# Kernel tuning notes

Measured on AMD Instinct MI355X. Metric: run time of the kernel, lower is better.

The kernel has to match this reference:

```python
import math
import jax, jax.numpy as jnp
import numpy as np

B, H, HKV, L, S, D = 1, 32, 8, 2048, 2048, 128
N_REP = H // HKV          # 4
SCALE = 1.0 / math.sqrt(D)


def setup_inputs() -> dict:
    key = jax.random.key(0)
    k1, k2, k3, k4 = jax.random.split(key, 4)
    query = jax.random.normal(k1, (B, H, L, D), dtype=jnp.float32)
    k_ = jax.random.normal(k2, (B, HKV, S, D), dtype=jnp.float32)
    v_ = jax.random.normal(k3, (B, HKV, S, D), dtype=jnp.float32)
    attn_mask = jax.random.normal(k4, (B, 1, L, S), dtype=jnp.float32)
    return {"query": query, "key": k_, "value": v_, "attn_mask": attn_mask}


def reference(query, key, value, attn_mask):
    # repeat_kv: Q -> [B, HKV, n_rep, L, D]; K/V stay [B, HKV, S, D]
    # (the torch code reshapes K/V to [B, HKV, 1, S, D]; broadcasting via
    # einsum is equivalent), mask unsqueezed at dim 1 -> [B, 1, 1, L, S].
    q = query.reshape(B, HKV, N_REP, L, D)
    scores = jnp.einsum("bkrld,bksd->bkrls", q, key)          # [B,HKV,n_rep,L,S]
    scores = scores + attn_mask[:, None]                        # broadcast add
    # softmax_fp8(x, dim=-1, invAttnHead=1/sqrt(D)) scales input by invAttnHead
    w = jax.nn.softmax(scores * SCALE, axis=-1)
    # dropout_p = 0.0 -> identity
    out = jnp.einsum("bkrls,bksd->bkrld", w, value)             # [B,HKV,n_rep,L,D]
    return out
```

## Files before the change

kernel.cpp:

```cpp
#include <hip/hip_runtime.h>

#define NH   32
#define NKV  8
#define LQ   2048
#define SK   2048
#define DH   128
#define BM   128
#define BN   64
#define KSTRIDE 136
#define VSTRIDE 72
#define PSTRIDE 72

typedef __attribute__((ext_vector_type(8)))  short bf8;
typedef __attribute__((ext_vector_type(4)))  float f4;
typedef __attribute__((ext_vector_type(16))) float f16v;

#if __has_builtin(__builtin_amdgcn_exp2f)
#define EXP2F(x) __builtin_amdgcn_exp2f(x)
#else
#define EXP2F(x) exp2f(x)
#endif

__device__ __forceinline__ unsigned short f2bf(float f) {
    unsigned int u = __builtin_bit_cast(unsigned int, f);
    u = (u + 0x7FFFu + ((u >> 16) & 1u)) >> 16;
    return (unsigned short)u;
}

__global__ __launch_bounds__(256) void convert_k_kernel(
    const float* __restrict__ K, unsigned short* __restrict__ Kb)
{
    size_t base = ((size_t)blockIdx.x * 256 + threadIdx.x) * 8;
    float4 a = *(const float4*)(K + base);
    float4 b = *(const float4*)(K + base + 4);
    bf8 o;
    o[0] = (short)f2bf(a.x); o[1] = (short)f2bf(a.y);
    o[2] = (short)f2bf(a.z); o[3] = (short)f2bf(a.w);
    o[4] = (short)f2bf(b.x); o[5] = (short)f2bf(b.y);
    o[6] = (short)f2bf(b.z); o[7] = (short)f2bf(b.w);
    *(bf8*)(Kb + base) = o;
}

__global__ __launch_bounds__(256) void transpose_v_kernel(
    const float* __restrict__ V, unsigned short* __restrict__ VTb)
{
    __shared__ __align__(16) unsigned short Vl[DH * VSTRIDE];
    const int tid = threadIdx.x;
    const int kv  = blockIdx.x >> 5;
    const int s0  = (blockIdx.x & 31) * 64;
    const float* Vh = V + (size_t)kv * SK * DH;

    #pragma unroll
    for (int i = 0; i < 8; ++i) {
        int idx = tid * 4 + i * 1024;
        int s = idx >> 7, d = idx & 127;
        const float4 v4 = *(const float4*)(Vh + (size_t)(s0 + s) * DH + d);
        Vl[(d + 0) * VSTRIDE + s] = f2bf(v4.x);
        Vl[(d + 1) * VSTRIDE + s] = f2bf(v4.y);
        Vl[(d + 2) * VSTRIDE + s] = f2bf(v4.z);
        Vl[(d + 3) * VSTRIDE + s] = f2bf(v4.w);
    }
    __syncthreads();
    unsigned short* out = VTb + (size_t)kv * DH * SK;
    #pragma unroll
    for (int i = 0; i < 4; ++i) {
        int c = tid + i * 256;
        int d = c >> 3, s8 = (c & 7) * 8;
        *(bf8*)(out + (size_t)d * SK + s0 + s8) = *(const bf8*)(Vl + d * VSTRIDE + s8);
    }
}

__global__ __launch_bounds__(256, 2) void fattn_kernel(
    const float* __restrict__ Q, const unsigned short* __restrict__ Kb,
    const unsigned short* __restrict__ VTb, const float* __restrict__ M,
    float* __restrict__ O)
{
    __shared__ __align__(16) unsigned short Klds[BN * KSTRIDE];
    __shared__ __align__(16) unsigned short Vlds[DH * VSTRIDE];
    __shared__ __align__(16) unsigned short Plds[4 * 32 * PSTRIDE];

    const int tid  = threadIdx.x;
    const int wave = tid >> 6;
    const int lane = tid & 63;
    const int l32  = lane & 31;
    const int hh   = lane >> 5;

    const int bx = blockIdx.x;
    const int h  = bx >> 4;
    const int lt = bx & 15;
    const int q0 = lt * BM;
    const int kv = h >> 2;

    const float*          Qh  = Q   + (size_t)h  * LQ * DH;
    const unsigned short* Kh  = Kb  + (size_t)kv * SK * DH;
    const unsigned short* VTh = VTb + (size_t)kv * DH * SK;

    const int sK0 = tid >> 4,        dK0 = (tid & 15) * 8;
    const int dV0 = tid >> 3,        sV0 = (tid & 7) * 8;

    const int qrow = q0 + wave * 32 + l32;
    const float* Mq = M + (size_t)qrow * SK;

    bf8 bQ[8];
    #pragma unroll
    for (int ks = 0; ks < 8; ++ks) {
        const float* qp = Qh + (size_t)qrow * DH + ks * 16 + hh * 8;
        float4 a = *(const float4*)(qp);
        float4 b = *(const float4*)(qp + 4);
        bQ[ks][0] = (short)f2bf(a.x); bQ[ks][1] = (short)f2bf(a.y);
        bQ[ks][2] = (short)f2bf(a.z); bQ[ks][3] = (short)f2bf(a.w);
        bQ[ks][4] = (short)f2bf(b.x); bQ[ks][5] = (short)f2bf(b.y);
        bQ[ks][6] = (short)f2bf(b.z); bQ[ks][7] = (short)f2bf(b.w);
    }

    f16v accO[4];
    #pragma unroll
    for (int nt = 0; nt < 4; ++nt)
        #pragma unroll
        for (int r = 0; r < 16; ++r) accO[nt][r] = 0.f;
    float lpart = 0.f;

    const float scale_log2e = 0.08838834764831845f * 1.4426950408889634f;

    unsigned short* Pw = Plds + wave * 32 * PSTRIDE;

    bf8 kf[4], vf[4];
    #pragma unroll
    for (int c = 0; c < 4; ++c) {
        kf[c] = *(const bf8*)(Kh + (size_t)(sK0 + c * 16) * DH + dK0);
        vf[c] = *(const bf8*)(VTh + (size_t)(dV0 + c * 32) * SK + sV0);
    }

    for (int s0i = 0; s0i < SK; s0i += BN) {
        __syncthreads();
        #pragma unroll
        for (int c = 0; c < 4; ++c) {
            *(bf8*)(Klds + (sK0 + c * 16) * KSTRIDE + dK0) = kf[c];
            *(bf8*)(Vlds + (dV0 + c * 32) * VSTRIDE + sV0) = vf[c];
        }
        __syncthreads();
        if (s0i + BN < SK) {
            #pragma unroll
            for (int c = 0; c < 4; ++c) {
                kf[c] = *(const bf8*)(Kh + (size_t)(s0i + BN + sK0 + c * 16) * DH + dK0);
                vf[c] = *(const bf8*)(VTh + (size_t)(dV0 + c * 32) * SK + s0i + BN + sV0);
            }
        }
        float4 mv[2][4];
        #pragma unroll
        for (int mt = 0; mt < 2; ++mt)
            #pragma unroll
            for (int grp = 0; grp < 4; ++grp)
                mv[mt][grp] = *(const float4*)(Mq + s0i + mt * 32 + grp * 8 + hh * 4);

        f16v accS[2];
        #pragma unroll
        for (int mt = 0; mt < 2; ++mt) {
            f16v a;
            #pragma unroll
            for (int r = 0; r < 16; ++r) a[r] = 0.f;
            #pragma unroll
            for (int ks = 0; ks < 8; ++ks) {
                bf8 aK = *(const bf8*)(Klds + (mt * 32 + l32) * KSTRIDE + ks * 16 + hh * 8);
                a = __builtin_amdgcn_mfma_f32_32x32x16_bf16(aK, bQ[ks], a, 0, 0, 0);
            }
            accS[mt] = a;
        }

        #pragma unroll
        for (int mt = 0; mt < 2; ++mt) {
            #pragma unroll
            for (int grp = 0; grp < 4; ++grp) {
                ushort4 pk;
                float e0 = EXP2F((accS[mt][grp * 4 + 0] + mv[mt][grp].x) * scale_log2e);
                float e1 = EXP2F((accS[mt][grp * 4 + 1] + mv[mt][grp].y) * scale_log2e);
                float e2 = EXP2F((accS[mt][grp * 4 + 2] + mv[mt][grp].z) * scale_log2e);
                float e3 = EXP2F((accS[mt][grp * 4 + 3] + mv[mt][grp].w) * scale_log2e);
                lpart += (e0 + e1) + (e2 + e3);
                pk.x = f2bf(e0); pk.y = f2bf(e1); pk.z = f2bf(e2); pk.w = f2bf(e3);
                *(ushort4*)(Pw + l32 * PSTRIDE + mt * 32 + grp * 8 + hh * 4) = pk;
            }
        }
        asm volatile("s_waitcnt lgkmcnt(0)" ::: "memory");

        bf8 bP[4];
        #pragma unroll
        for (int ks = 0; ks < 4; ++ks)
            bP[ks] = *(const bf8*)(Pw + l32 * PSTRIDE + ks * 16 + hh * 8);
        #pragma unroll
        for (int nt = 0; nt < 4; ++nt) {
            f16v a = accO[nt];
            #pragma unroll
            for (int ks = 0; ks < 4; ++ks) {
                bf8 aV = *(const bf8*)(Vlds + (nt * 32 + l32) * VSTRIDE + ks * 16 + hh * 8);
                a = __builtin_amdgcn_mfma_f32_32x32x16_bf16(aV, bP[ks], a, 0, 0, 0);
            }
            accO[nt] = a;
        }
    }

    float l = lpart + __shfl_xor(lpart, 32);
    float inv = 1.0f / l;
    float* Op = O + (size_t)h * LQ * DH + (size_t)qrow * DH;
    #pragma unroll
    for (int nt = 0; nt < 4; ++nt) {
        #pragma unroll
        for (int grp = 0; grp < 4; ++grp) {
            int d = nt * 32 + grp * 8 + hh * 4;
            float4 o;
            o.x = accO[nt][grp * 4 + 0] * inv;
            o.y = accO[nt][grp * 4 + 1] * inv;
            o.z = accO[nt][grp * 4 + 2] * inv;
            o.w = accO[nt][grp * 4 + 3] * inv;
            *(float4*)(Op + d) = o;
        }
    }
}

extern "C" void kernel_launch(void* const* d_in, const int* in_sizes, int n_in,
                              void* d_out, int out_size, void* d_ws, size_t ws_size,
                              hipStream_t stream) {
    const float* Q = (const float*)d_in[0];
    const float* K = (const float*)d_in[1];
    const float* V = (const float*)d_in[2];
    const float* M = (const float*)d_in[3];
    float* O = (float*)d_out;

    unsigned short* Kb  = (unsigned short*)d_ws;
    unsigned short* VTb = Kb + (size_t)NKV * SK * DH;

    convert_k_kernel<<<dim3((NKV * SK * DH) / (256 * 8)), 256, 0, stream>>>(K, Kb);
    transpose_v_kernel<<<dim3(NKV * (SK / 64)), 256, 0, stream>>>(V, VTb);

    dim3 grid(NH * (LQ / BM));
    fattn_kernel<<<grid, 256, 0, stream>>>(Q, Kb, VTb, M, O);
}
```

Measured before the change: 199.8 us.

## Rework attention kernel with async LDS double-buffering, swizzled layouts, register P

```diff
diff --git a/kernel.cpp b/kernel.cpp
--- a/kernel.cpp
+++ b/kernel.cpp
@@ -7,13 +7,12 @@
 #define DH   128
 #define BM   128
 #define BN   64
-#define KSTRIDE 136
+#define NT   (SK / BN)
 #define VSTRIDE 72
-#define PSTRIDE 72
 
 typedef __attribute__((ext_vector_type(8)))  short bf8;
-typedef __attribute__((ext_vector_type(4)))  float f4;
 typedef __attribute__((ext_vector_type(16))) float f16v;
+typedef __attribute__((ext_vector_type(4)))  unsigned int u32x4;
 
 #if __has_builtin(__builtin_amdgcn_exp2f)
 #define EXP2F(x) __builtin_amdgcn_exp2f(x)
@@ -27,18 +26,34 @@
     return (unsigned short)u;
 }
 
+__device__ __forceinline__ unsigned int cvtpk_bf16(float lo, float hi) {
+    unsigned int r;
+    asm("v_cvt_pk_bf16_f32 %0, %1, %2" : "=v"(r) : "v"(lo), "v"(hi));
+    return r;
+}
+
+#define GLOAD_LDS16(g, l)                                                      \
+    __builtin_amdgcn_global_load_lds(                                          \
+        (const __attribute__((address_space(1))) void*)(g),                    \
+        (__attribute__((address_space(3))) void*)(l), 16, 0, 0)
+
 __global__ __launch_bounds__(256) void convert_k_kernel(
     const float* __restrict__ K, unsigned short* __restrict__ Kb)
 {
-    size_t base = ((size_t)blockIdx.x * 256 + threadIdx.x) * 8;
-    float4 a = *(const float4*)(K + base);
-    float4 b = *(const float4*)(K + base + 4);
+    unsigned int cid = blockIdx.x * 256 + threadIdx.x;
+    unsigned int p   = cid & 15;
+    unsigned int row = cid >> 4;
+    unsigned int s   = row & (SK - 1);
+    unsigned int c   = p ^ (s & 15);
+    const float* src = K + (size_t)row * DH + c * 8;
+    float4 a = *(const float4*)(src);
+    float4 b = *(const float4*)(src + 4);
     bf8 o;
     o[0] = (short)f2bf(a.x); o[1] = (short)f2bf(a.y);
     o[2] = (short)f2bf(a.z); o[3] = (short)f2bf(a.w);
     o[4] = (short)f2bf(b.x); o[5] = (short)f2bf(b.y);
     o[6] = (short)f2bf(b.z); o[7] = (short)f2bf(b.w);
-    *(bf8*)(Kb + base) = o;
+    *(bf8*)(Kb + (size_t)row * DH + p * 8) = o;
 }
 
 __global__ __launch_bounds__(256) void transpose_v_kernel(
@@ -47,7 +62,8 @@
     __shared__ __align__(16) unsigned short Vl[DH * VSTRIDE];
     const int tid = threadIdx.x;
     const int kv  = blockIdx.x >> 5;
-    const int s0  = (blockIdx.x & 31) * 64;
+    const int t   = blockIdx.x & 31;
+    const int s0  = t * 64;
     const float* Vh = V + (size_t)kv * SK * DH;
 
     #pragma unroll
@@ -61,12 +77,13 @@
         Vl[(d + 3) * VSTRIDE + s] = f2bf(v4.w);
     }
     __syncthreads();
-    unsigned short* out = VTb + (size_t)kv * DH * SK;
+    unsigned short* out = VTb + (size_t)(kv * 32 + t) * (DH * 64);
     #pragma unroll
     for (int i = 0; i < 4; ++i) {
         int c = tid + i * 256;
-        int d = c >> 3, s8 = (c & 7) * 8;
-        *(bf8*)(out + (size_t)d * SK + s0 + s8) = *(const bf8*)(Vl + d * VSTRIDE + s8);
+        int d = c >> 3, p = c & 7;
+        int sc = (p ^ (d & 7)) * 8;
+        *(bf8*)(out + d * 64 + p * 8) = *(const bf8*)(Vl + d * VSTRIDE + sc);
     }
 }
 
@@ -75,144 +92,212 @@
     const unsigned short* __restrict__ VTb, const float* __restrict__ M,
     float* __restrict__ O)
 {
-    __shared__ __align__(16) unsigned short Klds[BN * KSTRIDE];
-    __shared__ __align__(16) unsigned short Vlds[DH * VSTRIDE];
-    __shared__ __align__(16) unsigned short Plds[4 * 32 * PSTRIDE];
+    __shared__ __align__(1024) unsigned char smem[65536];
+    unsigned char* KB = smem;
+    unsigned char* VB = smem + 32768;
 
     const int tid  = threadIdx.x;
     const int wave = tid >> 6;
     const int lane = tid & 63;
     const int l32  = lane & 31;
     const int hh   = lane >> 5;
-
-    const int bx = blockIdx.x;
+    const int qg   = wave >> 1;
+    const int sg   = wave & 1;
+
+    const int bx = ((int)blockIdx.x & 7) * 64 + ((int)blockIdx.x >> 3);
     const int h  = bx >> 4;
     const int lt = bx & 15;
     const int q0 = lt * BM;
     const int kv = h >> 2;
 
-    const float*          Qh  = Q   + (size_t)h  * LQ * DH;
-    const unsigned short* Kh  = Kb  + (size_t)kv * SK * DH;
-    const unsigned short* VTh = VTb + (size_t)kv * DH * SK;
-
-    const int sK0 = tid >> 4,        dK0 = (tid & 15) * 8;
-    const int dV0 = tid >> 3,        sV0 = (tid & 7) * 8;
-
-    const int qrow = q0 + wave * 32 + l32;
-    const float* Mq = M + (size_t)qrow * SK;
-
-    bf8 bQ[8];
-    #pragma unroll
-    for (int ks = 0; ks < 8; ++ks) {
-        const float* qp = Qh + (size_t)qrow * DH + ks * 16 + hh * 8;
-        float4 a = *(const float4*)(qp);
-        float4 b = *(const float4*)(qp + 4);
-        bQ[ks][0] = (short)f2bf(a.x); bQ[ks][1] = (short)f2bf(a.y);
-        bQ[ks][2] = (short)f2bf(a.z); bQ[ks][3] = (short)f2bf(a.w);
-        bQ[ks][4] = (short)f2bf(b.x); bQ[ks][5] = (short)f2bf(b.y);
-        bQ[ks][6] = (short)f2bf(b.z); bQ[ks][7] = (short)f2bf(b.w);
-    }
-
-    f16v accO[4];
-    #pragma unroll
-    for (int nt = 0; nt < 4; ++nt)
-        #pragma unroll
-        for (int r = 0; r < 16; ++r) accO[nt][r] = 0.f;
-    float lpart = 0.f;
-
-    const float scale_log2e = 0.08838834764831845f * 1.4426950408889634f;
-
-    unsigned short* Pw = Plds + wave * 32 * PSTRIDE;
-
-    bf8 kf[4], vf[4];
-    #pragma unroll
-    for (int c = 0; c < 4; ++c) {
-        kf[c] = *(const bf8*)(Kh + (size_t)(sK0 + c * 16) * DH + dK0);
-        vf[c] = *(const bf8*)(VTh + (size_t)(dV0 + c * 32) * SK + sV0);
-    }
-
-    for (int s0i = 0; s0i < SK; s0i += BN) {
-        __syncthreads();
-        #pragma unroll
-        for (int c = 0; c < 4; ++c) {
-            *(bf8*)(Klds + (sK0 + c * 16) * KSTRIDE + dK0) = kf[c];
-            *(bf8*)(Vlds + (dV0 + c * 32) * VSTRIDE + sV0) = vf[c];
-        }
-        __syncthreads();
-        if (s0i + BN < SK) {
-            #pragma unroll
-            for (int c = 0; c < 4; ++c) {
-                kf[c] = *(const bf8*)(Kh + (size_t)(s0i + BN + sK0 + c * 16) * DH + dK0);
-                vf[c] = *(const bf8*)(VTh + (size_t)(dV0 + c * 32) * SK + s0i + BN + sV0);
+    const float* Qh = Q + (size_t)h * LQ * DH;
+    const unsigned char* Kg = (const unsigned char*)(Kb  + (size_t)kv * SK * DH);
+    const unsigned char* Vg = (const unsigned char*)(VTb + (size_t)kv * SK * DH);
+
+    const int qrow0 = q0 + qg * 64 + l32;
+    const float* Mq0 = M + (size_t)qrow0 * SK;
+    const float* Mq1 = Mq0 + (size_t)32 * SK;
+
+    bf8 bQ[2][8];
+    #pragma unroll
+    for (int qt = 0; qt < 2; ++qt) {
+        const float* qp = Qh + (size_t)(qrow0 + qt * 32) * DH + hh * 8;
+        #pragma unroll
+        for (int ks = 0; ks < 8; ++ks) {
+            float4 a = *(const float4*)(qp + ks * 16);
+            float4 b = *(const float4*)(qp + ks * 16 + 4);
+            bf8 o;
+            o[0] = (short)f2bf(a.x); o[1] = (short)f2bf(a.y);
+            o[2] = (short)f2bf(a.z); o[3] = (short)f2bf(a.w);
+            o[4] = (short)f2bf(b.x); o[5] = (short)f2bf(b.y);
+            o[6] = (short)f2bf(b.z); o[7] = (short)f2bf(b.w);
+            bQ[qt][ks] = o;
+        }
+    }
+
+    const int krowz = (sg * 32 + l32) * 256 + ((hh * 16) ^ ((l32 & 15) << 4));
+    const int vrowz = l32 * 128 + ((sg * 64 + hh * 16) ^ ((l32 & 7) << 4));
+
+    const int stoff = wave * 4096 + lane * 16;
+
+    f16v accO[4][2];
+    #pragma unroll
+    for (int dt = 0; dt < 4; ++dt)
+        #pragma unroll
+        for (int qt = 0; qt < 2; ++qt)
+            #pragma unroll
+            for (int r = 0; r < 16; ++r) accO[dt][qt][r] = 0.f;
+    float lp0 = 0.f, lp1 = 0.f;
+    const float cl2e = 0.08838834764831845f * 1.4426950408889634f;
+
+    #pragma unroll
+    for (int c = 0; c < 4; ++c) GLOAD_LDS16(Kg + stoff + c * 1024, KB + stoff + c * 1024);
+    #pragma unroll
+    for (int c = 0; c < 4; ++c) GLOAD_LDS16(Vg + stoff + c * 1024, VB + stoff + c * 1024);
+
+    for (int t = 0; t < NT; ++t) {
+        const int cur = t & 1;
+
+        const float* mp0 = Mq0 + t * 64 + sg * 32 + hh * 4;
+        const float* mp1 = Mq1 + t * 64 + sg * 32 + hh * 4;
+        float4 mv0[4], mv1[4];
+        #pragma unroll
+        for (int g = 0; g < 4; ++g) mv0[g] = *(const float4*)(mp0 + g * 8);
+        #pragma unroll
+        for (int g = 0; g < 4; ++g) mv1[g] = *(const float4*)(mp1 + g * 8);
+        __builtin_amdgcn_sched_barrier(0);
+
+        {
+            const int tn = (t + 1) & (NT - 1);
+            const unsigned char* ksrc = Kg + (size_t)tn * 16384 + stoff;
+            const unsigned char* vsrc = Vg + (size_t)tn * 16384 + stoff;
+            unsigned char* kdst = KB + (cur ^ 1) * 16384 + stoff;
+            unsigned char* vdst = VB + (cur ^ 1) * 16384 + stoff;
+            #pragma unroll
+            for (int c = 0; c < 4; ++c) GLOAD_LDS16(ksrc + c * 1024, kdst + c * 1024);
+            #pragma unroll
+            for (int c = 0; c < 4; ++c) GLOAD_LDS16(vsrc + c * 1024, vdst + c * 1024);
+        }
+        __builtin_amdgcn_sched_barrier(0);
+        asm volatile("s_waitcnt vmcnt(16)" ::: "memory");
+        __builtin_amdgcn_s_barrier();
+        asm volatile("" ::: "memory");
+
+        const unsigned char* kb = KB + cur * 16384;
+        f16v s0, s1;
+        #pragma unroll
+        for (int r = 0; r < 16; ++r) { s0[r] = 0.f; s1[r] = 0.f; }
+        __builtin_amdgcn_s_setprio(1);
+        #pragma unroll
+        for (int ks = 0; ks < 8; ++ks) {
+            bf8 aK = *(const bf8*)(kb + (krowz ^ (ks << 5)));
+            s0 = __builtin_amdgcn_mfma_f32_32x32x16_bf16(aK, bQ[0][ks], s0, 0, 0, 0);
+            s1 = __builtin_amdgcn_mfma_f32_32x32x16_bf16(aK, bQ[1][ks], s1, 0, 0, 0);
+        }
+        __builtin_amdgcn_s_setprio(0);
+
+        unsigned int pk0[8], pk1[8];
+        #pragma unroll
+        for (int g = 0; g < 4; ++g) {
+            float e0 = EXP2F((s0[g*4+0] + mv0[g].x) * cl2e);
+            float e1 = EXP2F((s0[g*4+1] + mv0[g].y) * cl2e);
+            float e2 = EXP2F((s0[g*4+2] + mv0[g].z) * cl2e);
+            float e3 = EXP2F((s0[g*4+3] + mv0[g].w) * cl2e);
+            lp0 += (e0 + e1) + (e2 + e3);
+            pk0[g*2+0] = cvtpk_bf16(e0, e1);
+            pk0[g*2+1] = cvtpk_bf16(e2, e3);
+        }
+        #pragma unroll
+        for (int g = 0; g < 4; ++g) {
+            float e0 = EXP2F((s1[g*4+0] + mv1[g].x) * cl2e);
+            float e1 = EXP2F((s1[g*4+1] + mv1[g].y) * cl2e);
+            float e2 = EXP2F((s1[g*4+2] + mv1[g].z) * cl2e);
+            float e3 = EXP2F((s1[g*4+3] + mv1[g].w) * cl2e);
+            lp1 += (e0 + e1) + (e2 + e3);
+            pk1[g*2+0] = cvtpk_bf16(e0, e1);
+            pk1[g*2+1] = cvtpk_bf16(e2, e3);
+        }
+        bf8 bP0[2], bP1[2];
+        #pragma unroll
+        for (int ks = 0; ks < 2; ++ks) {
+            unsigned int a0 = pk0[4*ks+0], b0 = pk0[4*ks+2];
+            unsigned int a1 = pk0[4*ks+1], b1 = pk0[4*ks+3];
+            asm volatile("v_permlane32_swap_b32 %0, %1" : "+v"(a0), "+v"(b0));
+            asm volatile("v_permlane32_swap_b32 %0, %1" : "+v"(a1), "+v"(b1));
+            u32x4 w; w[0] = a0; w[1] = a1; w[2] = b0; w[3] = b1;
+            bP0[ks] = __builtin_bit_cast(bf8, w);
+            unsigned int c0 = pk1[4*ks+0], d0 = pk1[4*ks+2];
+            unsigned int c1 = pk1[4*ks+1], d1 = pk1[4*ks+3];
+            asm volatile("v_permlane32_swap_b32 %0, %1" : "+v"(c0), "+v"(d0));
+            asm volatile("v_permlane32_swap_b32 %0, %1" : "+v"(c1), "+v"(d1));
+            u32x4 w2; w2[0] = c0; w2[1] = c1; w2[2] = d0; w2[3] = d1;
+            bP1[ks] = __builtin_bit_cast(bf8, w2);
+        }
+
+        const unsigned char* vb = VB + cur * 16384;
+        __builtin_amdgcn_s_setprio(1);
+        #pragma unroll
+        for (int dt = 0; dt < 4; ++dt) {
+            #pragma unroll
+            for (int ks = 0; ks < 2; ++ks) {
+                bf8 aV = *(const bf8*)(vb + dt * 4096 + (vrowz ^ (ks << 5)));
+                accO[dt][0] = __builtin_amdgcn_mfma_f32_32x32x16_bf16(aV, bP0[ks], accO[dt][0], 0, 0, 0);
+                accO[dt][1] = __builtin_amdgcn_mfma_f32_32x32x16_bf16(aV, bP1[ks], accO[dt][1], 0, 0, 0);
             }
         }
-        float4 mv[2][4];
-        #pragma unroll
-        for (int mt = 0; mt < 2; ++mt)
-            #pragma unroll
-            for (int grp = 0; grp < 4; ++grp)
-                mv[mt][grp] = *(const float4*)(Mq + s0i + mt * 32 + grp * 8 + hh * 4);
-
-        f16v accS[2];
-        #pragma unroll
-        for (int mt = 0; mt < 2; ++mt) {
-            f16v a;
-            #pragma unroll
-            for (int r = 0; r < 16; ++r) a[r] = 0.f;
-            #pragma unroll
-            for (int ks = 0; ks < 8; ++ks) {
-                bf8 aK = *(const bf8*)(Klds + (mt * 32 + l32) * KSTRIDE + ks * 16 + hh * 8);
-                a = __builtin_amdgcn_mfma_f32_32x32x16_bf16(aK, bQ[ks], a, 0, 0, 0);
+        __builtin_amdgcn_s_setprio(0);
+        asm volatile("" ::: "memory");
+        __builtin_amdgcn_s_barrier();
+        asm volatile("" ::: "memory");
+    }
+
+    asm volatile("s_waitcnt vmcnt(0)" ::: "memory");
+    __builtin_amdgcn_s_barrier();
+    asm volatile("" ::: "memory");
+    float* xs  = (float*)smem;
+    float* lsc = (float*)(smem + 32768);
+    const int pw = qg * 2 + (sg ^ 1);
+    lsc[(wave * 2 + 0) * 64 + lane] = lp0;
+    lsc[(wave * 2 + 1) * 64 + lane] = lp1;
+    float lq[2];
+    float* Op0 = O + (size_t)h * LQ * DH + (size_t)qrow0 * DH;
+    #pragma unroll
+    for (int qt = 0; qt < 2; ++qt) {
+        #pragma unroll
+        for (int i = 0; i < 2; ++i) {
+            const int dt = (sg ^ 1) * 2 + i;
+            #pragma unroll
+            for (int r = 0; r < 16; ++r)
+                xs[((qg * 4 + dt) * 16 + r) * 64 + lane] = accO[dt][qt][r];
+        }
+        asm volatile("" ::: "memory");
+        __builtin_amdgcn_s_barrier();
+        asm volatile("" ::: "memory");
+        if (qt == 0) {
+            lq[0] = lp0 + lsc[(pw * 2 + 0) * 64 + lane];
+            lq[1] = lp1 + lsc[(pw * 2 + 1) * 64 + lane];
+            lq[0] += __shfl_xor(lq[0], 32);
+            lq[1] += __shfl_xor(lq[1], 32);
+        }
+        const float inv = 1.0f / lq[qt];
+        float* Op = Op0 + (size_t)qt * 32 * DH;
+        #pragma unroll
+        for (int i = 0; i < 2; ++i) {
+            const int dt = sg * 2 + i;
+            #pragma unroll
+            for (int g = 0; g < 4; ++g) {
+                float4 o;
+                o.x = (accO[dt][qt][g*4+0] + xs[((qg*4+dt)*16 + g*4+0)*64 + lane]) * inv;
+                o.y = (accO[dt][qt][g*4+1] + xs[((qg*4+dt)*16 + g*4+1)*64 + lane]) * inv;
+                o.z = (accO[dt][qt][g*4+2] + xs[((qg*4+dt)*16 + g*4+2)*64 + lane]) * inv;
+                o.w = (accO[dt][qt][g*4+3] + xs[((qg*4+dt)*16 + g*4+3)*64 + lane]) * inv;
+                *(float4*)(Op + dt * 32 + g * 8 + hh * 4) = o;
             }
-            accS[mt] = a;
-        }
-
-        #pragma unroll
-        for (int mt = 0; mt < 2; ++mt) {
-            #pragma unroll
-            for (int grp = 0; grp < 4; ++grp) {
-                ushort4 pk;
-                float e0 = EXP2F((accS[mt][grp * 4 + 0] + mv[mt][grp].x) * scale_log2e);
-                float e1 = EXP2F((accS[mt][grp * 4 + 1] + mv[mt][grp].y) * scale_log2e);
-                float e2 = EXP2F((accS[mt][grp * 4 + 2] + mv[mt][grp].z) * scale_log2e);
-                float e3 = EXP2F((accS[mt][grp * 4 + 3] + mv[mt][grp].w) * scale_log2e);
-                lpart += (e0 + e1) + (e2 + e3);
-                pk.x = f2bf(e0); pk.y = f2bf(e1); pk.z = f2bf(e2); pk.w = f2bf(e3);
-                *(ushort4*)(Pw + l32 * PSTRIDE + mt * 32 + grp * 8 + hh * 4) = pk;
-            }
-        }
-        asm volatile("s_waitcnt lgkmcnt(0)" ::: "memory");
-
-        bf8 bP[4];
-        #pragma unroll
-        for (int ks = 0; ks < 4; ++ks)
-            bP[ks] = *(const bf8*)(Pw + l32 * PSTRIDE + ks * 16 + hh * 8);
-        #pragma unroll
-        for (int nt = 0; nt < 4; ++nt) {
-            f16v a = accO[nt];
-            #pragma unroll
-            for (int ks = 0; ks < 4; ++ks) {
-                bf8 aV = *(const bf8*)(Vlds + (nt * 32 + l32) * VSTRIDE + ks * 16 + hh * 8);
-                a = __builtin_amdgcn_mfma_f32_32x32x16_bf16(aV, bP[ks], a, 0, 0, 0);
-            }
-            accO[nt] = a;
-        }
-    }
-
-    float l = lpart + __shfl_xor(lpart, 32);
-    float inv = 1.0f / l;
-    float* Op = O + (size_t)h * LQ * DH + (size_t)qrow * DH;
-    #pragma unroll
-    for (int nt = 0; nt < 4; ++nt) {
-        #pragma unroll
-        for (int grp = 0; grp < 4; ++grp) {
-            int d = nt * 32 + grp * 8 + hh * 4;
-            float4 o;
-            o.x = accO[nt][grp * 4 + 0] * inv;
-            o.y = accO[nt][grp * 4 + 1] * inv;
-            o.z = accO[nt][grp * 4 + 2] * inv;
-            o.w = accO[nt][grp * 4 + 3] * inv;
-            *(float4*)(Op + d) = o;
+        }
+        if (qt == 0) {
+            asm volatile("" ::: "memory");
+            __builtin_amdgcn_s_barrier();
+            asm volatile("" ::: "memory");
         }
     }
 }
@@ -229,7 +314,7 @@
     unsigned short* Kb  = (unsigned short*)d_ws;
     unsigned short* VTb = Kb + (size_t)NKV * SK * DH;
 
-    convert_k_kernel<<<dim3((NKV * SK * DH) / (256 * 8)), 256, 0, stream>>>(K, Kb);
+    convert_k_kernel<<<dim3((NKV * SK * 16) / 256), 256, 0, stream>>>(K, Kb);
     transpose_v_kernel<<<dim3(NKV * (SK / 64)), 256, 0, stream>>>(V, VTb);
 
     dim3 grid(NH * (LQ / BM));
```

Measured after the change: 410.2 us. +105.2%, slower.
